# Kernel tuning notes

Measured on AMD Instinct MI355X. Metric: run time of the kernel, lower is better.

## Reference

```python
import jax, jax.numpy as jnp
import numpy as np


def _gskan_layer(x, Lam, eps, a):
    # x: [B, n_in], Lam: [n_in, n_out], eps: [n_out], a: scalar PReLU weight
    s = x[:, :, None] + eps  # [B, n_in, n_out] broadcast add
    act = jnp.where(s >= 0, s, a * s)  # PReLU with single shared parameter
    return jnp.einsum('bpq,pq->bq', act, Lam)  # weighted sum over n_in


def setup_inputs() -> dict:
    key = jax.random.key(0)
    B, input_dim, width, depth, output_dim = 1024, 256, 512, 3, 256
    dims = [input_dim] + [width] * depth + [output_dim]
    ks = jax.random.split(key, 1 + 2 * (len(dims) - 1))
    inp = {"x": jax.random.normal(ks[0], (B, input_dim), dtype=jnp.float32)}
    for i in range(len(dims) - 1):
        n_in, n_out = dims[i], dims[i + 1]
        inp[f"L{i}_Lambda"] = 0.02 * jax.random.normal(ks[1 + 2 * i], (n_in, n_out), dtype=jnp.float32)
        inp[f"L{i}_eps"] = 0.02 * jax.random.normal(ks[2 + 2 * i], (n_out,), dtype=jnp.float32)
        inp[f"L{i}_a"] = jnp.float32(0.25)  # PReLU default init
    return inp


def reference(x,
              L0_Lambda, L0_eps, L0_a,
              L1_Lambda, L1_eps, L1_a,
              L2_Lambda, L2_eps, L2_a,
              L3_Lambda, L3_eps, L3_a):
    params = [(L0_Lambda, L0_eps, L0_a), (L1_Lambda, L1_eps, L1_a),
              (L2_Lambda, L2_eps, L2_a), (L3_Lambda, L3_eps, L3_a)]
    for Lam, eps, a in params:
        x = _gskan_layer(x, Lam, eps, a)
    return x
```

## Files before the change

### kernel.cpp

```cpp
#include <hip/hip_runtime.h>


#define PCHUNK 32
#define XS_STRIDE 36

__global__ __launch_bounds__(256) void gskan_partial_kernel(
    const float* __restrict__ X,
    const float* __restrict__ Lam,
    const float* __restrict__ Eps,
    const float* __restrict__ Aw,
    float* __restrict__ Part,
    int B, int n_in, int n_out, int p_per_split,
    int nq, int nb, int nsplit)
{
    __shared__ float xs[64 * XS_STRIDE];
    __shared__ float ls[PCHUNK * 64];

    int q_tile, b_tile, zsp;
    {
        const int g = blockIdx.x;
        const int per_z = nq * nb;
        if ((nsplit & 7) == 0 || nsplit * per_z == 1024) {
            const int cls = g & 7;
            const int idx = g >> 3;
            zsp    = cls + 8 * (idx / per_z);
            const int r = idx % per_z;
            q_tile = r % nq;
            b_tile = r / nq;
        } else {
            zsp    = g / per_z;
            const int r = g % per_z;
            q_tile = r % nq;
            b_tile = r / nq;
        }
    }

    const int tid = threadIdx.x;
    const int qg  = tid & 15;
    const int bl  = tid >> 4;

    const int q0 = q_tile * 64;
    const int b0 = b_tile * 64;
    const int p_begin = zsp * p_per_split;
    int p_end = p_begin + p_per_split;
    if (p_end > n_in) p_end = n_in;

    const float a  = Aw[0];
    const float c1 = 0.5f * (1.0f + a);
    const float c2 = 0.5f * (1.0f - a);

    const float4 ev = *reinterpret_cast<const float4*>(Eps + q0 + qg * 4);
    const float ee[4] = {ev.x, ev.y, ev.z, ev.w};

    float acc1[4][4] = {};
    float acc2[4][4] = {};

    const int srowX = tid >> 3, spgX = tid & 7;
    const int srowL = tid >> 4, sc4L = tid & 15;

    for (int pc = p_begin; pc < p_end; pc += PCHUNK) {
        #pragma unroll
        for (int r = 0; r < 2; ++r) {
            const int row = srowX + r * 32;
            float4 v = *reinterpret_cast<const float4*>(
                X + (size_t)(b0 + row) * n_in + pc + spgX * 4);
            *reinterpret_cast<float4*>(&xs[row * XS_STRIDE + spgX * 4]) = v;
        }
        #pragma unroll
        for (int r = 0; r < 2; ++r) {
            const int row = srowL + r * 16;
            float4 v = *reinterpret_cast<const float4*>(
                Lam + (size_t)(pc + row) * n_out + q0 + sc4L * 4);
            *reinterpret_cast<float4*>(&ls[row * 64 + sc4L * 4]) = v;
        }
        __syncthreads();

        #pragma unroll
        for (int p = 0; p < PCHUNK; p += 4) {
            float4 xv[4];
            #pragma unroll
            for (int i = 0; i < 4; ++i)
                xv[i] = *reinterpret_cast<const float4*>(&xs[(bl * 4 + i) * XS_STRIDE + p]);

            #pragma unroll
            for (int pp = 0; pp < 4; ++pp) {
                float4 lv = *reinterpret_cast<const float4*>(&ls[(p + pp) * 64 + qg * 4]);
                const float le[4] = {lv.x, lv.y, lv.z, lv.w};
                #pragma unroll
                for (int i = 0; i < 4; ++i) {
                    const float xe = (pp == 0) ? xv[i].x :
                                     (pp == 1) ? xv[i].y :
                                     (pp == 2) ? xv[i].z : xv[i].w;
                    #pragma unroll
                    for (int j = 0; j < 4; ++j) {
                        const float s = xe + ee[j];
                        acc1[i][j] = fmaf(s,        le[j], acc1[i][j]);
                        acc2[i][j] = fmaf(fabsf(s), le[j], acc2[i][j]);
                    }
                }
            }
        }
        __syncthreads();
    }

    float* P = Part + (size_t)zsp * B * n_out;
    #pragma unroll
    for (int i = 0; i < 4; ++i) {
        const int b = b0 + bl * 4 + i;
        float4 o;
        o.x = c1 * acc1[i][0] + c2 * acc2[i][0];
        o.y = c1 * acc1[i][1] + c2 * acc2[i][1];
        o.z = c1 * acc1[i][2] + c2 * acc2[i][2];
        o.w = c1 * acc1[i][3] + c2 * acc2[i][3];
        *reinterpret_cast<float4*>(P + (size_t)b * n_out + q0 + qg * 4) = o;
    }
}

__global__ __launch_bounds__(256) void gskan_combine_kernel(
    const float* __restrict__ Part, float* __restrict__ Y, int n, int nsplit)
{
    int i = (blockIdx.x * 256 + threadIdx.x) * 4;
    if (i >= n) return;
    float4 acc = *reinterpret_cast<const float4*>(Part + i);
    for (int s = 1; s < nsplit; ++s) {
        float4 v = *reinterpret_cast<const float4*>(Part + (size_t)s * n + i);
        acc.x += v.x; acc.y += v.y; acc.z += v.z; acc.w += v.w;
    }
    *reinterpret_cast<float4*>(Y + i) = acc;
}

extern "C" void kernel_launch(void* const* d_in, const int* in_sizes, int n_in_args,
                              void* d_out, int out_size, void* d_ws, size_t ws_size,
                              hipStream_t stream)
{
    (void)n_in_args; (void)out_size;

    const float* x = (const float*)d_in[0];

    struct LayerP { const float *Lam, *Eps, *Aw; int n_in, n_out; };
    LayerP layers[4];
    for (int i = 0; i < 4; ++i) {
        layers[i].Lam   = (const float*)d_in[1 + 3 * i];
        layers[i].Eps   = (const float*)d_in[2 + 3 * i];
        layers[i].Aw    = (const float*)d_in[3 + 3 * i];
        layers[i].n_out = in_sizes[2 + 3 * i];
        layers[i].n_in  = in_sizes[1 + 3 * i] / layers[i].n_out;
    }
    const int B = in_sizes[0] / layers[0].n_in;

    char* ws = (char*)d_ws;
    float* Part = (float*)ws;
    float* yA   = (float*)(ws + (size_t)(16u << 20));
    float* yB   = (float*)(ws + (size_t)(18u << 20));
    const bool have_ws = ws_size >= (size_t)(20u << 20);

    const float* cur = x;
    for (int i = 0; i < 4; ++i) {
        const LayerP& ly = layers[i];
        const int nq = ly.n_out / 64;
        const int nb = B / 64;

        int nsplit = 1;
        if (have_ws) {
            nsplit = 1024 / (nq * nb);
            if (nsplit < 1) nsplit = 1;
            int max_split = ly.n_in / PCHUNK;
            if (nsplit > max_split) nsplit = max_split;
        }
        int p_per = ((ly.n_in + nsplit * PCHUNK - 1) / (nsplit * PCHUNK)) * PCHUNK;
        nsplit = (ly.n_in + p_per - 1) / p_per;

        while ((size_t)nsplit * B * ly.n_out * 4 > ((size_t)16u << 20)) nsplit--;
        if (nsplit < 1) nsplit = 1;
        p_per = ((ly.n_in + nsplit * PCHUNK - 1) / (nsplit * PCHUNK)) * PCHUNK;
        nsplit = (ly.n_in + p_per - 1) / p_per;

        float* Y = (i == 3) ? (float*)d_out : ((i % 2 == 0) ? yA : yB);
        float* dst = (nsplit == 1) ? Y : Part;

        dim3 grid(nq * nb * nsplit), block(256);
        hipLaunchKernelGGL(gskan_partial_kernel, grid, block, 0, stream,
                           cur, ly.Lam, ly.Eps, ly.Aw, dst,
                           B, ly.n_in, ly.n_out, p_per, nq, nb, nsplit);

        if (nsplit > 1) {
            const int n = B * ly.n_out;
            dim3 cg((n / 4 + 255) / 256), cb(256);
            hipLaunchKernelGGL(gskan_combine_kernel, cg, cb, 0, stream, Part, Y, n, nsplit);
        }
        cur = Y;
    }
}
```

Measured before the change: 123.7 us.

## Double-buffer shared-memory tiles with register prefetch of next chunk

```diff
diff --git a/kernel.cpp b/kernel.cpp
--- a/kernel.cpp
+++ b/kernel.cpp
@@ -13,8 +13,8 @@
     int B, int n_in, int n_out, int p_per_split,
     int nq, int nb, int nsplit)
 {
-    __shared__ float xs[64 * XS_STRIDE];
-    __shared__ float ls[PCHUNK * 64];
+    __shared__ float xs[2][64 * XS_STRIDE];
+    __shared__ float ls[2][PCHUNK * 64];
 
     int q_tile, b_tile, zsp;
     {
@@ -58,33 +58,51 @@
     const int srowX = tid >> 3, spgX = tid & 7;
     const int srowL = tid >> 4, sc4L = tid & 15;
 
-    for (int pc = p_begin; pc < p_end; pc += PCHUNK) {
-        #pragma unroll
-        for (int r = 0; r < 2; ++r) {
-            const int row = srowX + r * 32;
-            float4 v = *reinterpret_cast<const float4*>(
-                X + (size_t)(b0 + row) * n_in + pc + spgX * 4);
-            *reinterpret_cast<float4*>(&xs[row * XS_STRIDE + spgX * 4]) = v;
-        }
-        #pragma unroll
-        for (int r = 0; r < 2; ++r) {
-            const int row = srowL + r * 16;
-            float4 v = *reinterpret_cast<const float4*>(
-                Lam + (size_t)(pc + row) * n_out + q0 + sc4L * 4);
-            *reinterpret_cast<float4*>(&ls[row * 64 + sc4L * 4]) = v;
-        }
-        __syncthreads();
-
+    const float* Xr0 = X + (size_t)(b0 + srowX) * n_in + spgX * 4;
+    const float* Xr1 = X + (size_t)(b0 + srowX + 32) * n_in + spgX * 4;
+    const float* Lr0 = Lam + (size_t)srowL * n_out + q0 + sc4L * 4;
+    const float* Lr1 = Lam + (size_t)(srowL + 16) * n_out + q0 + sc4L * 4;
+
+    {
+        const int pc = p_begin;
+        float4 v0 = *reinterpret_cast<const float4*>(Xr0 + pc);
+        float4 v1 = *reinterpret_cast<const float4*>(Xr1 + pc);
+        float4 l0 = *reinterpret_cast<const float4*>(Lr0 + (size_t)pc * n_out);
+        float4 l1 = *reinterpret_cast<const float4*>(Lr1 + (size_t)pc * n_out);
+        *reinterpret_cast<float4*>(&xs[0][srowX * XS_STRIDE + spgX * 4]) = v0;
+        *reinterpret_cast<float4*>(&xs[0][(srowX + 32) * XS_STRIDE + spgX * 4]) = v1;
+        *reinterpret_cast<float4*>(&ls[0][srowL * 64 + sc4L * 4]) = l0;
+        *reinterpret_cast<float4*>(&ls[0][(srowL + 16) * 64 + sc4L * 4]) = l1;
+    }
+    __syncthreads();
+
+    for (int c = 0;; ++c) {
+        const int pc_next = p_begin + (c + 1) * PCHUNK;
+        const bool hasnext = pc_next < p_end;
+
+        float4 nx0, nx1, nl0, nl1;
+        if (hasnext) {
+            nx0 = *reinterpret_cast<const float4*>(Xr0 + pc_next);
+            nx1 = *reinterpret_cast<const float4*>(Xr1 + pc_next);
+            nl0 = *reinterpret_cast<const float4*>(Lr0 + (size_t)pc_next * n_out);
+            nl1 = *reinterpret_cast<const float4*>(Lr1 + (size_t)pc_next * n_out);
+        }
+        __builtin_amdgcn_sched_barrier(0);
+
+        const float* xcur = xs[c & 1];
+        const float* lcur = ls[c & 1];
         #pragma unroll
         for (int p = 0; p < PCHUNK; p += 4) {
             float4 xv[4];
             #pragma unroll
             for (int i = 0; i < 4; ++i)
-                xv[i] = *reinterpret_cast<const float4*>(&xs[(bl * 4 + i) * XS_STRIDE + p]);
+                xv[i] = *reinterpret_cast<const float4*>(
+                    &xcur[(bl * 4 + i) * XS_STRIDE + p]);
 
             #pragma unroll
             for (int pp = 0; pp < 4; ++pp) {
-                float4 lv = *reinterpret_cast<const float4*>(&ls[(p + pp) * 64 + qg * 4]);
+                float4 lv = *reinterpret_cast<const float4*>(
+                    &lcur[(p + pp) * 64 + qg * 4]);
                 const float le[4] = {lv.x, lv.y, lv.z, lv.w};
                 #pragma unroll
                 for (int i = 0; i < 4; ++i) {
@@ -100,6 +118,13 @@
                 }
             }
         }
+
+        if (!hasnext) break;
+        const int nxt = (c + 1) & 1;
+        *reinterpret_cast<float4*>(&xs[nxt][srowX * XS_STRIDE + spgX * 4]) = nx0;
+        *reinterpret_cast<float4*>(&xs[nxt][(srowX + 32) * XS_STRIDE + spgX * 4]) = nx1;
+        *reinterpret_cast<float4*>(&ls[nxt][srowL * 64 + sc4L * 4]) = nl0;
+        *reinterpret_cast<float4*>(&ls[nxt][(srowL + 16) * 64 + sc4L * 4]) = nl1;
         __syncthreads();
     }
 
```

After: 169.4 us. 1.37x slower.
